# Performance work log

Measured on AMD Instinct MI355X. Metric: run time of the kernel, lower is better.

## Reference

```python
import jax, jax.numpy as jnp
import numpy as np
import math

D_MODEL = 1024
NUM_HEADS = 16
DK = D_MODEL // NUM_HEADS
THETA = 10000.0


def _rope(x, cos, sin):
    # x: (..., S, dk); cos/sin: (S, dk//2). Interleaved (even/odd) rotation,
    # matching x1=x[...,0::2], x2=x[...,1::2] then re-interleave via stack.
    x1 = x[..., 0::2]
    x2 = x[..., 1::2]
    r1 = x1 * cos - x2 * sin
    r2 = x1 * sin + x2 * cos
    return jnp.stack((r1, r2), axis=-1).reshape(x.shape)


def setup_inputs() -> dict:
    key = jax.random.key(0)
    k1, k2, k3 = jax.random.split(key, 3)
    B, S = 2, 2048
    x = jax.random.normal(k1, (B, S, D_MODEL), dtype=jnp.float32)
    std_qkv = (2.0 / (D_MODEL + 3 * D_MODEL)) ** 0.5
    Wqkv = jax.random.normal(k2, (3 * D_MODEL, D_MODEL), dtype=jnp.float32) * std_qkv
    std_o = (2.0 / (D_MODEL + D_MODEL)) ** 0.5
    Wo = jax.random.normal(k3, (D_MODEL, D_MODEL), dtype=jnp.float32) * std_o
    return {"x": x, "Wqkv": Wqkv, "Wo": Wo}


def reference(x, Wqkv, Wo):
    B, S, D = x.shape
    # fused QKV projection: Linear stores W as (out, in), y = x @ W^T
    qkv = jnp.einsum('bsd,od->bso', x, Wqkv)  # (B, S, 3*D)
    # split order in the source rearrange is (three, numheads, dk)
    qkv = qkv.reshape(B, S, 3, NUM_HEADS, DK).transpose(2, 0, 3, 1, 4)  # (3,B,H,S,dk)
    q, k, v = qkv[0], qkv[1], qkv[2]

    # RoPE tables (registered buffers in the source, deterministic constants)
    inv_freqs = 1.0 / (THETA ** (jnp.arange(0, DK, 2, dtype=jnp.float32) / DK))
    t = jnp.arange(S, dtype=jnp.float32)
    freqs = t[:, None] * inv_freqs[None, :]  # (S, dk//2)
    cos, sin = jnp.cos(freqs), jnp.sin(freqs)
    q = _rope(q, cos, sin)
    k = _rope(k, cos, sin)

    # naive full-materialization causal attention
    scores = jnp.einsum('bhqd,bhkd->bhqk', q, k) / math.sqrt(DK)  # (B,H,S,S)
    causal = jnp.tril(jnp.ones((S, S), dtype=bool))
    scores = jnp.where(causal, scores, -jnp.inf)
    attn = jax.nn.softmax(scores, axis=-1)
    out = jnp.einsum('bhqk,bhkd->bhqd', attn, v)  # (B,H,S,dk)
    out = out.transpose(0, 2, 1, 3).reshape(B, S, D)  # concat heads
    return jnp.einsum('bsd,od->bso', out, Wo)
```

## Files before the change

### kernel.cpp

```cpp
#include <hip/hip_runtime.h>
#include <hip/hip_bf16.h>
#include <cstdint>
#include <cstddef>


typedef unsigned short u16;
typedef unsigned int   u32;

typedef float f32x4 __attribute__((ext_vector_type(4)));
typedef short frag_t __attribute__((ext_vector_type(8)));

__device__ __forceinline__ f32x4 mfma16(frag_t a, frag_t b, f32x4 c) {
  return __builtin_amdgcn_mfma_f32_16x16x32_bf16(a, b, c, 0, 0, 0);
}

typedef __attribute__((address_space(1))) void as1_void;
typedef __attribute__((address_space(3))) void as3_void;
__device__ __forceinline__ void gload_lds16(const void* g, void* l) {
  __builtin_amdgcn_global_load_lds((as1_void*)g, (as3_void*)l, 16, 0, 0);
}

__device__ __forceinline__ u16 f2bf(float f) {
  u32 u = __builtin_bit_cast(u32, f);
  u += 0x7fffu + ((u >> 16) & 1u);
  return (u16)(u >> 16);
}
__device__ __forceinline__ float bf2f(u16 h) {
  u32 u = ((u32)h) << 16;
  return __builtin_bit_cast(float, u);
}
__device__ __forceinline__ u16 bf16u(float f) {
  __hip_bfloat16 h = __float2bfloat16(f);
  u16 u;
  __builtin_memcpy(&u, &h, 2);
  return u;
}
__device__ __forceinline__ float exp2_hw(float x) {
  float r;
  asm("v_exp_f32 %0, %1" : "=v"(r) : "v"(x));
  return r;
}

static constexpr int Bb = 2, Ss = 2048, Hh = 16, Dd = 1024;
static constexpr int Mm = Bb * Ss;
static constexpr int NT = Ss / 64;

__global__ __launch_bounds__(256) void cvt_f32_bf16(const float* __restrict__ in,
                                                    u16* __restrict__ out, int n4) {
  for (int i = blockIdx.x * blockDim.x + threadIdx.x; i < n4;
       i += gridDim.x * blockDim.x) {
    float4 v = ((const float4*)in)[i];
    ushort4 o;
    o.x = f2bf(v.x); o.y = f2bf(v.y); o.z = f2bf(v.z); o.w = f2bf(v.w);
    ((ushort4*)out)[i] = o;
  }
}

__global__ __launch_bounds__(256) void build_rope_table(float2* __restrict__ tab) {
  int i = blockIdx.x * blockDim.x + threadIdx.x;
  if (i >= Ss * 32) return;
  int s = i >> 5, j = i & 31;
  const float log2_theta_over_32 = 0.41524101186091903f;
  float inv = exp2f(-(float)j * log2_theta_over_32);
  float fr = (float)s * inv;
  float sn, cs;
  sincosf(fr, &sn, &cs);
  tab[i] = make_float2(cs, sn);
}

template <bool OUT_BF16>
__global__ __launch_bounds__(256) void gemm_bt_kernel(const u16* __restrict__ A,
                                                      const u16* __restrict__ Bm,
                                                      void* __restrict__ Cv,
                                                      int Mdim, int Ndim, int Kdim) {
  __shared__ __align__(16) u16 As[2][128 * 64];
  __shared__ __align__(16) u16 Bs[2][128 * 64];
  const int tid = threadIdx.x;
  const int lane = tid & 63, wid = tid >> 6;
  const int wr = wid >> 1, wc = wid & 1;
  const int lr = lane & 15, lg = lane >> 4;

  const int nwg = gridDim.x * gridDim.y;
  const int orig = blockIdx.y * gridDim.x + blockIdx.x;
  const int cpx = nwg >> 3;
  const int swz = (orig & 7) * cpx + (orig >> 3);
  const int bx = swz % gridDim.x, by = swz / gridDim.x;
  const int m0 = by * 128, n0 = bx * 128;

  f32x4 acc[4][4] = {};

  const int rowA = lane >> 3;
  const int colu = ((lane & 7) ^ rowA) * 8;

  auto stage = [&](int buf, int kt) {
#pragma unroll
    for (int i = 0; i < 4; i++) {
      int chunk = wid * 4 + i;
      const u16* ga = A + (size_t)(m0 + chunk * 8 + rowA) * Kdim + kt + colu;
      gload_lds16(ga, &As[buf][chunk * 512]);
      const u16* gb = Bm + (size_t)(n0 + chunk * 8 + rowA) * Kdim + kt + colu;
      gload_lds16(gb, &Bs[buf][chunk * 512]);
    }
  };

  const int niter = Kdim >> 6;

  stage(0, 0);
  stage(1, 64);
  asm volatile("s_waitcnt vmcnt(8)" ::: "memory");
  __builtin_amdgcn_sched_barrier(0);
  __builtin_amdgcn_s_barrier();
  __builtin_amdgcn_sched_barrier(0);

  const int rsw = (lr & 7) * 8;
  int cur = 0;
  for (int it = 0; it < niter; ++it) {
#pragma unroll
    for (int ks = 0; ks < 2; ks++) {
      frag_t a[4], b[4];
#pragma unroll
      for (int mt = 0; mt < 4; mt++)
        a[mt] = *(const frag_t*)&As[cur][(wr * 64 + mt * 16 + lr) * 64 +
                                         ((ks * 32 + lg * 8) ^ rsw)];
#pragma unroll
      for (int nt = 0; nt < 4; nt++)
        b[nt] = *(const frag_t*)&Bs[cur][(wc * 64 + nt * 16 + lr) * 64 +
                                         ((ks * 32 + lg * 8) ^ rsw)];
#pragma unroll
      for (int mt = 0; mt < 4; mt++)
#pragma unroll
        for (int nt = 0; nt < 4; nt++)
          acc[mt][nt] = mfma16(a[mt], b[nt], acc[mt][nt]);
    }

    if (it + 1 < niter) {
      __builtin_amdgcn_s_barrier();
      __builtin_amdgcn_sched_barrier(0);
      if (it + 2 < niter) {
        stage(cur, (it + 2) << 6);
        asm volatile("s_waitcnt vmcnt(8)" ::: "memory");
      } else {
        asm volatile("s_waitcnt vmcnt(0)" ::: "memory");
      }
      __builtin_amdgcn_sched_barrier(0);
      __builtin_amdgcn_s_barrier();
      __builtin_amdgcn_sched_barrier(0);
      cur ^= 1;
    }
  }

#pragma unroll
  for (int mt = 0; mt < 4; mt++)
#pragma unroll
    for (int nt = 0; nt < 4; nt++)
#pragma unroll
      for (int r = 0; r < 4; r++) {
        size_t row = (size_t)(m0 + wr * 64 + mt * 16 + lg * 4 + r);
        size_t col = (size_t)(n0 + wc * 64 + nt * 16 + lr);
        if (OUT_BF16)
          ((u16*)Cv)[row * Ndim + col] = f2bf(acc[mt][nt][r]);
        else
          ((float*)Cv)[row * Ndim + col] = acc[mt][nt][r];
      }
}

__global__ __launch_bounds__(256) void rope_kernel(const u16* __restrict__ qkv,
                                                   const float2* __restrict__ tab,
                                                   u16* __restrict__ q_r,
                                                   u16* __restrict__ k_r,
                                                   u16* __restrict__ vt) {
  const int bh = blockIdx.y, b = bh >> 4, h = bh & 15;
  const int s0 = blockIdx.x * 64;
  const int t = threadIdx.x;
  __shared__ __align__(16) u16 Vls[64 * 72];

  const int srow = t >> 2, c4 = t & 3;
  const int s = s0 + srow;
  const size_t rowbase = (size_t)(b * Ss + s) * 3072 + h * 64 + c4 * 16;

  u16 xq[16] __attribute__((aligned(16)));
  u16 xk[16] __attribute__((aligned(16)));
  u16 xv[16] __attribute__((aligned(16)));
  *(uint4*)&xq[0] = *(const uint4*)(qkv + rowbase);
  *(uint4*)&xq[8] = *(const uint4*)(qkv + rowbase + 8);
  *(uint4*)&xk[0] = *(const uint4*)(qkv + rowbase + 1024);
  *(uint4*)&xk[8] = *(const uint4*)(qkv + rowbase + 1024 + 8);
  *(uint4*)&xv[0] = *(const uint4*)(qkv + rowbase + 2048);
  *(uint4*)&xv[8] = *(const uint4*)(qkv + rowbase + 2048 + 8);

  u16 oq[16] __attribute__((aligned(16)));
  u16 ok[16] __attribute__((aligned(16)));
  const int j0 = c4 * 8;
  const float qscale = 0.125f * 1.4426950408889634f;
#pragma unroll
  for (int p = 0; p < 8; p++) {
    float2 cs = tab[s * 32 + j0 + p];
    float q1 = bf2f(xq[2 * p]), q2 = bf2f(xq[2 * p + 1]);
    float k1 = bf2f(xk[2 * p]), k2 = bf2f(xk[2 * p + 1]);
    oq[2 * p]     = f2bf((q1 * cs.x - q2 * cs.y) * qscale);
    oq[2 * p + 1] = f2bf((q1 * cs.y + q2 * cs.x) * qscale);
    ok[2 * p]     = f2bf(k1 * cs.x - k2 * cs.y);
    ok[2 * p + 1] = f2bf(k1 * cs.y + k2 * cs.x);
  }
  const size_t obase = ((size_t)bh * Ss + s) * 64 + c4 * 16;
  *(uint4*)(q_r + obase)     = *(uint4*)&oq[0];
  *(uint4*)(q_r + obase + 8) = *(uint4*)&oq[8];
  *(uint4*)(k_r + obase)     = *(uint4*)&ok[0];
  *(uint4*)(k_r + obase + 8) = *(uint4*)&ok[8];

  *(uint4*)&Vls[srow * 72 + c4 * 16]     = *(uint4*)&xv[0];
  *(uint4*)&Vls[srow * 72 + c4 * 16 + 8] = *(uint4*)&xv[8];
  __syncthreads();
  const int d = t >> 2, cq = t & 3;
  u16 ov[16] __attribute__((aligned(16)));
#pragma unroll
  for (int i = 0; i < 16; i++) ov[i] = Vls[(cq * 16 + i) * 72 + d];
  const size_t vbase = ((size_t)bh * 64 + d) * Ss + s0 + cq * 16;
  *(uint4*)(vt + vbase)     = *(uint4*)&ov[0];
  *(uint4*)(vt + vbase + 8) = *(uint4*)&ov[8];
}

__global__ __launch_bounds__(512, 4) void attn_kernel(const u16* __restrict__ q_r,
                                                      const u16* __restrict__ k_r,
                                                      const u16* __restrict__ vt,
                                                      u16* __restrict__ o) {
  const int pr = blockIdx.x;
  const int bh = blockIdx.y;
  const int b = bh >> 4, h = bh & 15;
  const int tid = threadIdx.x;
  const int lane = tid & 63, w = tid >> 6;
  const int ww = w & 3;
  const int lr = lane & 15, lg = lane >> 4;

  const int qt = (w < 4) ? pr : (NT - 1 - pr);
  const int qtB = NT - 1 - pr;

  __shared__ __align__(16) u16 Ks[2][64 * 72];
  __shared__ __align__(16) u16 Vs[2][64 * 72];
  __shared__ __align__(16) u16 Ps[8][16 * 72];

  const size_t kvbase = (size_t)bh * Ss * 64;
  const size_t vtbase = (size_t)bh * 64 * Ss;
  u16* Pw = &Ps[w][0];
  const int qrow = ww * 16 + lr;

  frag_t q0f, q1f;
  {
    const u16* qa = q_r + kvbase + (size_t)(qt * 64 + qrow) * 64 + lg * 8;
    q0f = *(const frag_t*)qa;
    q1f = *(const frag_t*)(qa + 32);
  }

  const int srow = tid >> 3, scol = (tid & 7) * 8;
  uint4 kreg, vreg;
  const u16* kp = k_r + kvbase;
  const u16* vp = vt + vtbase;

  auto issue = [&](int kt) {
    kreg = *(const uint4*)(kp + (size_t)(kt * 64 + srow) * 64 + scol);
    vreg = *(const uint4*)(vp + (size_t)srow * Ss + kt * 64 + scol);
  };
  auto commit = [&](int buf) {
    *(uint4*)&Ks[buf][srow * 72 + scol] = kreg;
    *(uint4*)&Vs[buf][srow * 72 + scol] = vreg;
  };

  f32x4 oacc[4] = {};
  float l_run = 0.f;

  issue(0);
  commit(0);
  __syncthreads();

  for (int kt = 0; kt <= qtB; kt++) {
    const int cur = kt & 1;
    const bool last = (kt == qtB);
    if (!last) issue(kt + 1);

    if (kt <= qt) {
      f32x4 sa[4];
      __builtin_amdgcn_s_setprio(1);
#pragma unroll
      for (int kf = 0; kf < 4; kf++) {
        frag_t k0 = *(const frag_t*)&Ks[cur][(kf * 16 + lr) * 72 + lg * 8];
        frag_t k1 = *(const frag_t*)&Ks[cur][(kf * 16 + lr) * 72 + 32 + lg * 8];
        sa[kf] = mfma16(k0, q0f, f32x4{0.f, 0.f, 0.f, 0.f});
        sa[kf] = mfma16(k1, q1f, sa[kf]);
      }
      __builtin_amdgcn_s_setprio(0);

      if (kt == qt) {
#pragma unroll
        for (int kf = 0; kf < 4; kf++)
#pragma unroll
          for (int r = 0; r < 4; r++)
            if (kf * 16 + lg * 4 + r > qrow) sa[kf][r] = -1e30f;
      }

      float ls = 0.f;
#pragma unroll
      for (int kf = 0; kf < 4; kf++) {
        float p0 = exp2_hw(sa[kf][0]), p1 = exp2_hw(sa[kf][1]);
        float p2 = exp2_hw(sa[kf][2]), p3 = exp2_hw(sa[kf][3]);
        ls += (p0 + p1) + (p2 + p3);
        ushort4 w4;
        w4.x = bf16u(p0); w4.y = bf16u(p1); w4.z = bf16u(p2); w4.w = bf16u(p3);
        *(ushort4*)&Pw[lr * 72 + kf * 16 + lg * 4] = w4;
      }
      l_run += ls;

      __builtin_amdgcn_s_setprio(1);
#pragma unroll
      for (int ks = 0; ks < 2; ks++) {
        frag_t pa = *(const frag_t*)&Pw[lr * 72 + ks * 32 + lg * 8];
#pragma unroll
        for (int df = 0; df < 4; df++) {
          frag_t bv = *(const frag_t*)&Vs[cur][(df * 16 + lr) * 72 + ks * 32 + lg * 8];
          oacc[df] = mfma16(pa, bv, oacc[df]);
        }
      }
      __builtin_amdgcn_s_setprio(0);
    }

    if (!last) commit(cur ^ 1);
    __syncthreads();
  }

  l_run += __shfl_xor(l_run, 16);
  l_run += __shfl_xor(l_run, 32);
#pragma unroll
  for (int r = 0; r < 4; r++) {
    float il = 1.0f / __shfl(l_run, lg * 4 + r);
    size_t row = (size_t)b * Ss + qt * 64 + ww * 16 + lg * 4 + r;
#pragma unroll
    for (int df = 0; df < 4; df++)
      o[row * 1024 + h * 64 + df * 16 + lr] = f2bf(oacc[df][r] * il);
  }
}

extern "C" void kernel_launch(void* const* d_in, const int* in_sizes, int n_in,
                              void* d_out, int out_size, void* d_ws, size_t ws_size,
                              hipStream_t stream) {
  const float* x    = (const float*)d_in[0];
  const float* Wqkv = (const float*)d_in[1];
  const float* Wo   = (const float*)d_in[2];
  float* out = (float*)d_out;
  char* ws = (char*)d_ws;

  constexpr size_t TAB_OFF  = 0;
  constexpr size_t XB_OFF   = TAB_OFF + 524288;
  constexpr size_t WQB_OFF  = XB_OFF + 8388608;
  constexpr size_t WOB_OFF  = WQB_OFF + 6291456;
  constexpr size_t QKV_OFF  = WOB_OFF + 2097152;
  constexpr size_t QR_OFF   = QKV_OFF + 25165824;
  constexpr size_t KR_OFF   = QR_OFF + 8388608;
  constexpr size_t VT_OFF   = KR_OFF + 8388608;
  constexpr size_t AO_OFF   = VT_OFF + 8388608;

  float2* tab = (float2*)(ws + TAB_OFF);
  u16* xb     = (u16*)(ws + XB_OFF);
  u16* wqkvb  = (u16*)(ws + WQB_OFF);
  u16* wob    = (u16*)(ws + WOB_OFF);
  u16* qkv    = (u16*)(ws + QKV_OFF);
  u16* q_r    = (u16*)(ws + QR_OFF);
  u16* k_r    = (u16*)(ws + KR_OFF);
  u16* vt     = (u16*)(ws + VT_OFF);
  u16* ao     = (u16*)(ws + AO_OFF);

  build_rope_table<<<256, 256, 0, stream>>>(tab);
  cvt_f32_bf16<<<2048, 256, 0, stream>>>(x, xb, Mm * Dd / 4);
  cvt_f32_bf16<<<1536, 256, 0, stream>>>(Wqkv, wqkvb, 3 * Dd * Dd / 4);
  cvt_f32_bf16<<<512, 256, 0, stream>>>(Wo, wob, Dd * Dd / 4);

  gemm_bt_kernel<true><<<dim3(3 * Dd / 128, Mm / 128), 256, 0, stream>>>(
      xb, wqkvb, qkv, Mm, 3 * Dd, Dd);

  rope_kernel<<<dim3(Ss / 64, Bb * Hh), 256, 0, stream>>>(qkv, tab, q_r, k_r, vt);

  attn_kernel<<<dim3(NT / 2, Bb * Hh), 512, 0, stream>>>(q_r, k_r, vt, ao);

  gemm_bt_kernel<false><<<dim3(Dd / 128, Mm / 128), 256, 0, stream>>>(
      ao, wob, out, Mm, Dd, Dd);
}
```

Baseline: 131.7 us.

## Split paired attention blocks into per-tile blocks with XOR-swizzled LDS

The attention kernel no longer pairs a short and a long causal query tile in one 512-thread block. It now launches one 256-thread block per query tile, ordered longest-first, and each block loops only over its own KV tiles. LDS padding (stride 72) is replaced by an XOR swizzle on 8-element groups with stride 64, which shrinks shared memory while aiming to avoid bank conflicts. This gives up the built-in load balance of pairing tiles in exchange for no idle waves per block and smaller blocks, relying on the hardware scheduler to balance the uneven work.

```diff
diff --git a/kernel.cpp b/kernel.cpp
--- a/kernel.cpp
+++ b/kernel.cpp
@@ -220,29 +220,26 @@
   *(uint4*)(vt + vbase + 8) = *(uint4*)&ov[8];
 }
 
-__global__ __launch_bounds__(512, 4) void attn_kernel(const u16* __restrict__ q_r,
+__global__ __launch_bounds__(256, 4) void attn_kernel(const u16* __restrict__ q_r,
                                                       const u16* __restrict__ k_r,
                                                       const u16* __restrict__ vt,
                                                       u16* __restrict__ o) {
-  const int pr = blockIdx.x;
+  const int qt = NT - 1 - blockIdx.x;
   const int bh = blockIdx.y;
   const int b = bh >> 4, h = bh & 15;
   const int tid = threadIdx.x;
   const int lane = tid & 63, w = tid >> 6;
-  const int ww = w & 3;
   const int lr = lane & 15, lg = lane >> 4;
 
-  const int qt = (w < 4) ? pr : (NT - 1 - pr);
-  const int qtB = NT - 1 - pr;
-
-  __shared__ __align__(16) u16 Ks[2][64 * 72];
-  __shared__ __align__(16) u16 Vs[2][64 * 72];
-  __shared__ __align__(16) u16 Ps[8][16 * 72];
+  __shared__ __align__(16) u16 Ks[2][64 * 64];
+  __shared__ __align__(16) u16 Vs[2][64 * 64];
+  __shared__ __align__(16) u16 Ps[4][16 * 64];
 
   const size_t kvbase = (size_t)bh * Ss * 64;
   const size_t vtbase = (size_t)bh * 64 * Ss;
   u16* Pw = &Ps[w][0];
-  const int qrow = ww * 16 + lr;
+  const int qrow = w * 16 + lr;
+  const int sw = lr & 7;
 
   frag_t q0f, q1f;
   {
@@ -251,18 +248,25 @@
     q1f = *(const frag_t*)(qa + 32);
   }
 
-  const int srow = tid >> 3, scol = (tid & 7) * 8;
-  uint4 kreg, vreg;
+  const int srow0 = tid >> 3, srow1 = srow0 + 32;
+  const int sgr = tid & 7;
+  const int scolg = (sgr * 8);
+  const int scols = ((sgr ^ (srow0 & 7)) * 8);
+  uint4 kreg[2], vreg[2];
   const u16* kp = k_r + kvbase;
   const u16* vp = vt + vtbase;
 
   auto issue = [&](int kt) {
-    kreg = *(const uint4*)(kp + (size_t)(kt * 64 + srow) * 64 + scol);
-    vreg = *(const uint4*)(vp + (size_t)srow * Ss + kt * 64 + scol);
+    kreg[0] = *(const uint4*)(kp + (size_t)(kt * 64 + srow0) * 64 + scolg);
+    kreg[1] = *(const uint4*)(kp + (size_t)(kt * 64 + srow1) * 64 + scolg);
+    vreg[0] = *(const uint4*)(vp + (size_t)srow0 * Ss + kt * 64 + scolg);
+    vreg[1] = *(const uint4*)(vp + (size_t)srow1 * Ss + kt * 64 + scolg);
   };
   auto commit = [&](int buf) {
-    *(uint4*)&Ks[buf][srow * 72 + scol] = kreg;
-    *(uint4*)&Vs[buf][srow * 72 + scol] = vreg;
+    *(uint4*)&Ks[buf][srow0 * 64 + scols] = kreg[0];
+    *(uint4*)&Ks[buf][srow1 * 64 + scols] = kreg[1];
+    *(uint4*)&Vs[buf][srow0 * 64 + scols] = vreg[0];
+    *(uint4*)&Vs[buf][srow1 * 64 + scols] = vreg[1];
   };
 
   f32x4 oacc[4] = {};
@@ -272,55 +276,55 @@
   commit(0);
   __syncthreads();
 
-  for (int kt = 0; kt <= qtB; kt++) {
+  for (int kt = 0; kt <= qt; kt++) {
     const int cur = kt & 1;
-    const bool last = (kt == qtB);
+    const bool last = (kt == qt);
     if (!last) issue(kt + 1);
 
-    if (kt <= qt) {
-      f32x4 sa[4];
-      __builtin_amdgcn_s_setprio(1);
-#pragma unroll
-      for (int kf = 0; kf < 4; kf++) {
-        frag_t k0 = *(const frag_t*)&Ks[cur][(kf * 16 + lr) * 72 + lg * 8];
-        frag_t k1 = *(const frag_t*)&Ks[cur][(kf * 16 + lr) * 72 + 32 + lg * 8];
-        sa[kf] = mfma16(k0, q0f, f32x4{0.f, 0.f, 0.f, 0.f});
-        sa[kf] = mfma16(k1, q1f, sa[kf]);
+    f32x4 sa[4];
+    __builtin_amdgcn_s_setprio(1);
+#pragma unroll
+    for (int kf = 0; kf < 4; kf++) {
+      frag_t k0 = *(const frag_t*)&Ks[cur][(kf * 16 + lr) * 64 + ((lg ^ sw) * 8)];
+      frag_t k1 = *(const frag_t*)&Ks[cur][(kf * 16 + lr) * 64 + (((4 + lg) ^ sw) * 8)];
+      sa[kf] = mfma16(k0, q0f, f32x4{0.f, 0.f, 0.f, 0.f});
+      sa[kf] = mfma16(k1, q1f, sa[kf]);
+    }
+    __builtin_amdgcn_s_setprio(0);
+
+    if (last) {
+#pragma unroll
+      for (int kf = 0; kf < 4; kf++)
+#pragma unroll
+        for (int r = 0; r < 4; r++)
+          if (kf * 16 + lg * 4 + r > qrow) sa[kf][r] = -1e30f;
+    }
+
+    float ls = 0.f;
+#pragma unroll
+    for (int kf = 0; kf < 4; kf++) {
+      float p0 = exp2_hw(sa[kf][0]), p1 = exp2_hw(sa[kf][1]);
+      float p2 = exp2_hw(sa[kf][2]), p3 = exp2_hw(sa[kf][3]);
+      ls += (p0 + p1) + (p2 + p3);
+      ushort4 w4;
+      w4.x = bf16u(p0); w4.y = bf16u(p1); w4.z = bf16u(p2); w4.w = bf16u(p3);
+      const int pg = (kf * 2 + (lg >> 1)) ^ sw;
+      *(ushort4*)&Pw[lr * 64 + pg * 8 + (lg & 1) * 4] = w4;
+    }
+    l_run += ls;
+
+    __builtin_amdgcn_s_setprio(1);
+#pragma unroll
+    for (int ks = 0; ks < 2; ks++) {
+      frag_t pa = *(const frag_t*)&Pw[lr * 64 + (((ks * 4 + lg) ^ sw) * 8)];
+#pragma unroll
+      for (int df = 0; df < 4; df++) {
+        frag_t bv = *(const frag_t*)&Vs[cur][(df * 16 + lr) * 64 +
+                                             (((ks * 4 + lg) ^ sw) * 8)];
+        oacc[df] = mfma16(pa, bv, oacc[df]);
       }
-      __builtin_amdgcn_s_setprio(0);
-
-      if (kt == qt) {
-#pragma unroll
-        for (int kf = 0; kf < 4; kf++)
-#pragma unroll
-          for (int r = 0; r < 4; r++)
-            if (kf * 16 + lg * 4 + r > qrow) sa[kf][r] = -1e30f;
-      }
-
-      float ls = 0.f;
-#pragma unroll
-      for (int kf = 0; kf < 4; kf++) {
-        float p0 = exp2_hw(sa[kf][0]), p1 = exp2_hw(sa[kf][1]);
-        float p2 = exp2_hw(sa[kf][2]), p3 = exp2_hw(sa[kf][3]);
-        ls += (p0 + p1) + (p2 + p3);
-        ushort4 w4;
-        w4.x = bf16u(p0); w4.y = bf16u(p1); w4.z = bf16u(p2); w4.w = bf16u(p3);
-        *(ushort4*)&Pw[lr * 72 + kf * 16 + lg * 4] = w4;
-      }
-      l_run += ls;
-
-      __builtin_amdgcn_s_setprio(1);
-#pragma unroll
-      for (int ks = 0; ks < 2; ks++) {
-        frag_t pa = *(const frag_t*)&Pw[lr * 72 + ks * 32 + lg * 8];
-#pragma unroll
-        for (int df = 0; df < 4; df++) {
-          frag_t bv = *(const frag_t*)&Vs[cur][(df * 16 + lr) * 72 + ks * 32 + lg * 8];
-          oacc[df] = mfma16(pa, bv, oacc[df]);
-        }
-      }
-      __builtin_amdgcn_s_setprio(0);
-    }
+    }
+    __builtin_amdgcn_s_setprio(0);
 
     if (!last) commit(cur ^ 1);
     __syncthreads();
@@ -331,7 +335,7 @@
 #pragma unroll
   for (int r = 0; r < 4; r++) {
     float il = 1.0f / __shfl(l_run, lg * 4 + r);
-    size_t row = (size_t)b * Ss + qt * 64 + ww * 16 + lg * 4 + r;
+    size_t row = (size_t)b * Ss + qt * 64 + w * 16 + lg * 4 + r;
 #pragma unroll
     for (int df = 0; df < 4; df++)
       o[row * 1024 + h * 64 + df * 16 + lr] = f2bf(oacc[df][r] * il);
@@ -377,7 +381,7 @@
 
   rope_kernel<<<dim3(Ss / 64, Bb * Hh), 256, 0, stream>>>(qkv, tab, q_r, k_r, vt);
 
-  attn_kernel<<<dim3(NT / 2, Bb * Hh), 512, 0, stream>>>(q_r, k_r, vt, ao);
+  attn_kernel<<<dim3(NT, Bb * Hh), 256, 0, stream>>>(q_r, k_r, vt, ao);
 
   gemm_bt_kernel<false><<<dim3(Dd / 128, Mm / 128), 256, 0, stream>>>(
       ao, wob, out, Mm, Dd, Dd);
```

After: 210.8 us. 1.6x slower.
